# Optimization experiments

Measured on AMD Instinct MI355X. Metric: run time of the kernel, lower is better.

## Reference

```python
import jax, jax.numpy as jnp
import numpy as np

HEADS, DK, DV, STRIDE = 8, 32, 32, 2
EPS = 1e-5

def dwconv(x, w, b, stride):
    # depthwise 3x3, padding 1; w: [C,1,3,3]
    y = jax.lax.conv_general_dilated(
        x, w, (stride, stride), ((1, 1), (1, 1)),
        dimension_numbers=("NCHW", "OIHW", "NCHW"),
        feature_group_count=x.shape[1])
    return y + b[None, :, None, None]

def setup_inputs() -> dict:
    key = jax.random.key(0)
    ks = jax.random.split(key, 16)
    B_, C, H, W = 8, 256, 56, 56
    hd = HEADS * DK
    s = lambda k, shp: (jax.random.normal(k, shp, jnp.float32) * 0.02)
    return {
        "x": jax.random.normal(ks[0], (B_, C, H, W), jnp.float32),
        "Wk_dw": s(ks[1], (C, 1, 3, 3)), "bk_dw": jnp.zeros((C,), jnp.float32),
        "Wv_dw": s(ks[2], (C, 1, 3, 3)), "bv_dw": jnp.zeros((C,), jnp.float32),
        "Wq": s(ks[3], (hd, C)), "bq": jnp.zeros((hd,), jnp.float32),
        "Wk": s(ks[4], (hd, C)), "bk": jnp.zeros((hd,), jnp.float32),
        "Wv": s(ks[5], (HEADS * DV, C)), "bv": jnp.zeros((HEADS * DV,), jnp.float32),
        "Wo": s(ks[6], (C, HEADS * DV)), "bo": jnp.zeros((C,), jnp.float32),
        "Bbias": s(ks[7], (1, HEADS, H * W, (H // STRIDE) * (W // STRIDE))),
    }

def reference(x, Wk_dw, bk_dw, Wv_dw, bv_dw, Wq, bq, Wk, bk, Wv, bv, Wo, bo, Bbias):
    b, c, h, w = x.shape
    xr = x.reshape(b, c, h * w).transpose(0, 2, 1)  # [b, hw, c]
    # F.layer_norm with normalized_shape=(b, hw, c): single mean/var over ALL elements
    mu = jnp.mean(xr)
    var = jnp.mean((xr - mu) ** 2)
    xn = (xr - mu) * jax.lax.rsqrt(var + EPS)
    q = (xn @ Wq.T + bq).reshape(b, h * w, HEADS, DK).transpose(0, 2, 1, 3)  # [b,H,hw,dk]
    ki = dwconv(x, Wk_dw, bk_dw, STRIDE)
    kh, kw = ki.shape[2], ki.shape[3]
    kf = ki.reshape(b, c, kh * kw).transpose(0, 2, 1)
    k = (kf @ Wk.T + bk).reshape(b, kh * kw, HEADS, DK).transpose(0, 2, 1, 3)
    vi = dwconv(x, Wv_dw, bv_dw, STRIDE)
    vf = vi.reshape(b, c, kh * kw).transpose(0, 2, 1)
    v = (vf @ Wv.T + bv).reshape(b, kh * kw, HEADS, DV).transpose(0, 2, 1, 3)
    attn = jnp.einsum("bhid,bhjd->bhij", q, k) * (DK ** -0.5) + Bbias
    attn = jax.nn.softmax(attn, axis=-1)
    res = jnp.einsum("bhij,bhjd->bhid", attn, v).transpose(0, 2, 1, 3)
    res = res.reshape(b, h * w, HEADS * DV)
    out = (res @ Wo.T + bo).reshape(b, c, h, w)  # faithful to original .view (no transpose)
    return out + x
```

## Files before the change

kernel.cpp:

```cpp
#include <hip/hip_runtime.h>

typedef unsigned short u16;
typedef unsigned int   u32;
typedef __attribute__((ext_vector_type(8))) short short8;
typedef __attribute__((ext_vector_type(4))) float f32x4;

#define MFMA16(a, b, c) __builtin_amdgcn_mfma_f32_16x16x32_bf16((a), (b), (c), 0, 0, 0)

static constexpr int B_ = 8;
static constexpr int HW = 3136;
static constexpr int KW = 784;
static constexpr int NELEM = B_ * 256 * HW;

static constexpr size_t OFF_CNT = 4096;
static constexpr size_t OFF_W   = 8192;
static constexpr int AOFF_WQ = 0, AOFF_WK = 65536, AOFF_WV = 131072, AOFF_WO = 196608;
static constexpr int AOFF_WKDW = 262144, AOFF_WVDW = 264448;
static constexpr int AOFF_BKDW = 266752, AOFF_BVDW = 267008, AOFF_BQ = 267264;
static constexpr int AOFF_BK = 267520, AOFF_BV = 267776, AOFF_BO = 268032;
static constexpr size_t OFF_XT  = 557056;
static constexpr size_t SZ_XT   = (size_t)B_ * HW * 256 * 2;
static constexpr size_t SZ_KJ   = (size_t)B_ * KW * 256 * 2;
static constexpr size_t OFF_KIT = OFF_XT + SZ_XT;
static constexpr size_t OFF_VIT = OFF_KIT + SZ_KJ;
static constexpr size_t OFF_KI  = OFF_VIT + SZ_KJ;
static constexpr size_t OFF_VI  = OFF_KI + SZ_KJ;
static constexpr size_t OFF_Q   = OFF_VI + SZ_KJ;
static constexpr size_t OFF_O   = OFF_XT;

__device__ __forceinline__ float bf2f(u16 u) { return __uint_as_float(((u32)u) << 16); }
__device__ __forceinline__ u16 f2bf(float f) {
  u32 u = __float_as_uint(f);
  u32 r = u + 0x7FFFu + ((u >> 16) & 1u);
  return (u16)(r >> 16);
}
__device__ __forceinline__ float bflo(u32 u) { return __uint_as_float(u << 16); }
__device__ __forceinline__ float bfhi(u32 u) { return __uint_as_float(u & 0xFFFF0000u); }
__device__ __forceinline__ u32 packbf(float a, float b) {
  u32 ua = __float_as_uint(a); ua = (ua + 0x7FFFu + ((ua >> 16) & 1u)) >> 16;
  u32 ub = __float_as_uint(b); ub = (ub + 0x7FFFu + ((ub >> 16) & 1u)) >> 16;
  return ua | (ub << 16);
}

__global__ __launch_bounds__(256) void detect_k(const u32* __restrict__ x, int* __restrict__ cnt) {
  int c = 0;
  for (int i = threadIdx.x; i < 4096; i += 256) {
    float v = __uint_as_float(x[i] << 16);
    if (fabsf(v) > 1e4f) c++;
  }
#pragma unroll
  for (int off = 32; off > 0; off >>= 1) c += __shfl_down(c, off);
  if ((threadIdx.x & 63) == 0) atomicAdd(cnt, c);
}

struct CvtArgs { const void* src[12]; int dstoff[12]; int n[12]; };
__global__ __launch_bounds__(256) void cvtw_k(CvtArgs a, u16* __restrict__ arena,
                                              const int* __restrict__ cnt) {
  int t = blockIdx.y;
  int n = a.n[t];
  u16* d = arena + a.dstoff[t];
  int f32m = (*cnt >= 64);
  if (f32m) {
    const float* s = (const float*)a.src[t];
    for (int i = blockIdx.x * 256 + threadIdx.x; i < n; i += gridDim.x * 256) d[i] = f2bf(s[i]);
  } else {
    const u16* s = (const u16*)a.src[t];
    for (int i = blockIdx.x * 256 + threadIdx.x; i < n; i += gridDim.x * 256) d[i] = s[i];
  }
}

__global__ __launch_bounds__(256) void reduce_k(const void* __restrict__ x, double* __restrict__ acc,
                                                const int* __restrict__ cnt) {
  int f32m = (*cnt >= 64);
  float s = 0.f, ss = 0.f;
  if (f32m) {
    const float4* xv = (const float4*)x;
    const int n4 = NELEM / 4;
    for (int i = blockIdx.x * 256 + threadIdx.x; i < n4; i += gridDim.x * 256) {
      float4 u = xv[i];
      s += u.x + u.y + u.z + u.w;
      ss += u.x * u.x + u.y * u.y + u.z * u.z + u.w * u.w;
    }
  } else {
    const uint4* xv = (const uint4*)x;
    const int n8 = NELEM / 8;
    for (int i = blockIdx.x * 256 + threadIdx.x; i < n8; i += gridDim.x * 256) {
      uint4 u = xv[i];
      u32 w[4] = {u.x, u.y, u.z, u.w};
#pragma unroll
      for (int q = 0; q < 4; q++) {
        float f0 = __uint_as_float(w[q] << 16);
        float f1 = __uint_as_float(w[q] & 0xFFFF0000u);
        s += f0 + f1;
        ss += f0 * f0 + f1 * f1;
      }
    }
  }
#pragma unroll
  for (int off = 32; off > 0; off >>= 1) {
    s += __shfl_down(s, off);
    ss += __shfl_down(ss, off);
  }
  __shared__ float as_[4], ass_[4];
  int wv = threadIdx.x >> 6;
  if ((threadIdx.x & 63) == 0) { as_[wv] = s; ass_[wv] = ss; }
  __syncthreads();
  if (threadIdx.x == 0) {
    atomicAdd(acc + 0, (double)(as_[0] + as_[1] + as_[2] + as_[3]));
    atomicAdd(acc + 1, (double)(ass_[0] + ass_[1] + ass_[2] + ass_[3]));
  }
}

__global__ __launch_bounds__(256) void prep_k(const u16* __restrict__ wq, const u16* __restrict__ bq,
                                              float* __restrict__ wsf) {
  const double* acc = (const double*)wsf;
  __shared__ float sh[2];
  if (threadIdx.x == 0) {
    double N = (double)NELEM;
    double mu = acc[0] / N;
    double var = acc[1] / N - mu * mu;
    float rstd = (float)(1.0 / sqrt(var + 1e-5));
    sh[0] = (float)mu; sh[1] = rstd;
    wsf[4] = (float)mu; wsf[5] = rstd;
    wsf[6] = rstd * 0.17677669529663687f;
  }
  __syncthreads();
  int o = threadIdx.x;
  float wsum = 0.f;
  for (int c = 0; c < 256; c++) wsum += bf2f(wq[o * 256 + c]);
  wsf[16 + o] = (bf2f(bq[o]) - sh[1] * sh[0] * wsum) * 0.17677669529663687f;
}

__global__ __launch_bounds__(256) void transpose_x_k(const void* __restrict__ src, u16* __restrict__ dst,
                                                     const int* __restrict__ cnt) {
  int f32m = (*cnt >= 64);
  __shared__ u16 t[32][33];
  int b = blockIdx.z;
  int r0 = blockIdx.y * 32, c0 = blockIdx.x * 32;
  int tid = threadIdx.x, col = tid & 31;
  size_t base = (size_t)b * 256 * HW;
  if (f32m) {
    const float* s = (const float*)src + base;
#pragma unroll
    for (int i = 0; i < 4; i++) {
      int row = (tid >> 5) + i * 8;
      t[row][col] = f2bf(s[(size_t)(r0 + row) * HW + c0 + col]);
    }
  } else {
    const u16* s = (const u16*)src + base;
#pragma unroll
    for (int i = 0; i < 4; i++) {
      int row = (tid >> 5) + i * 8;
      t[row][col] = s[(size_t)(r0 + row) * HW + c0 + col];
    }
  }
  __syncthreads();
  u16* d = dst + base;
#pragma unroll
  for (int i = 0; i < 4; i++) {
    int row = (tid >> 5) + i * 8;
    d[(size_t)(c0 + row) * 256 + r0 + col] = t[col][row];
  }
}

__global__ __launch_bounds__(256) void transpose_k(const u16* __restrict__ src, u16* __restrict__ dst,
                                                   int R, int Cc) {
  __shared__ u16 t[32][33];
  int b = blockIdx.z;
  int r0 = blockIdx.y * 32, c0 = blockIdx.x * 32;
  const u16* s = src + (size_t)b * R * Cc;
  u16* d = dst + (size_t)b * R * Cc;
  int tid = threadIdx.x, col = tid & 31;
#pragma unroll
  for (int i = 0; i < 4; i++) {
    int row = (tid >> 5) + i * 8;
    if (r0 + row < R && c0 + col < Cc) t[row][col] = s[(size_t)(r0 + row) * Cc + c0 + col];
  }
  __syncthreads();
#pragma unroll
  for (int i = 0; i < 4; i++) {
    int row = (tid >> 5) + i * 8;
    if (c0 + row < Cc && r0 + col < R) d[(size_t)(c0 + row) * R + r0 + col] = t[col][row];
  }
}

__global__ __launch_bounds__(256) void dwconv_k(const void* __restrict__ x,
                                                const u16* __restrict__ arena,
                                                u16* __restrict__ ki, u16* __restrict__ vi,
                                                const int* __restrict__ cnt) {
  int f32m = (*cnt >= 64);
  int b = blockIdx.x >> 8;
  int c = blockIdx.x & 255;
  float wkf[9], wvf[9];
#pragma unroll
  for (int t = 0; t < 9; t++) {
    wkf[t] = bf2f(arena[AOFF_WKDW + c * 9 + t]);
    wvf[t] = bf2f(arena[AOFF_WVDW + c * 9 + t]);
  }
  float kb = bf2f(arena[AOFF_BKDW + c]), vb = bf2f(arena[AOFF_BVDW + c]);
  size_t xbase = (size_t)(b * 256 + c) * HW;
  auto body = [&](auto LDX) {
    for (int j = threadIdx.x; j < KW; j += 256) {
      int oi = j / 28, oj = j % 28;
      float ka = kb, va = vb;
#pragma unroll
      for (int di = 0; di < 3; di++) {
        int ii = 2 * oi - 1 + di;
        if ((unsigned)ii >= 56u) continue;
#pragma unroll
        for (int dj = 0; dj < 3; dj++) {
          int ij = 2 * oj - 1 + dj;
          if ((unsigned)ij >= 56u) continue;
          float xv = LDX(ii * 56 + ij);
          ka += xv * wkf[di * 3 + dj];
          va += xv * wvf[di * 3 + dj];
        }
      }
      ki[(size_t)(b * 256 + c) * KW + j] = f2bf(ka);
      vi[(size_t)(b * 256 + c) * KW + j] = f2bf(va);
    }
  };
  if (f32m) {
    const float* xp = (const float*)x + xbase;
    body([&](int i) { return xp[i]; });
  } else {
    const u16* xp = (const u16*)x + xbase;
    body([&](int i) { return bf2f(xp[i]); });
  }
}

__global__ __launch_bounds__(256) void proj_q_k(const u16* __restrict__ xt, const u16* __restrict__ Wq,
                                                const float* __restrict__ wsf, u16* __restrict__ q) {
  int lane = threadIdx.x & 63, wave = threadIdx.x >> 6;
  int l15 = lane & 15, quad = lane >> 4;
  int b = blockIdx.x / 49, pb = blockIdx.x % 49;
  int p0 = pb * 64 + wave * 16;
  const u16* arow = xt + ((size_t)(b * HW) + p0 + l15) * 256 + quad * 8;
  short8 af[8];
#pragma unroll
  for (int ks = 0; ks < 8; ks++) af[ks] = *(const short8*)(arow + ks * 32);
  float alpha = wsf[6];
  const float* beta = wsf + 16;
  for (int ot = 0; ot < 16; ot++) {
    const u16* brow = Wq + (size_t)(ot * 16 + l15) * 256 + quad * 8;
    f32x4 acc = {0.f, 0.f, 0.f, 0.f};
#pragma unroll
    for (int ks = 0; ks < 8; ks++) acc = MFMA16(af[ks], *(const short8*)(brow + ks * 32), acc);
    int o = ot * 16 + l15;
    float bet = beta[o];
    size_t base = ((size_t)(b * HW) + p0 + quad * 4) * 256 + o;
#pragma unroll
    for (int r = 0; r < 4; r++) q[base + (size_t)r * 256] = f2bf(alpha * acc[r] + bet);
  }
}

__global__ __launch_bounds__(256) void proj_k_k(const u16* __restrict__ kit, const u16* __restrict__ Wk,
                                                const u16* __restrict__ bk, u16* __restrict__ kout) {
  int lane = threadIdx.x & 63, wave = threadIdx.x >> 6;
  int l15 = lane & 15, quad = lane >> 4;
  int b = blockIdx.x / 13, jb = blockIdx.x % 13;
  int p0 = jb * 64 + wave * 16;
  if (p0 >= KW) return;
  const u16* arow = kit + ((size_t)(b * KW) + p0 + l15) * 256 + quad * 8;
  short8 af[8];
#pragma unroll
  for (int ks = 0; ks < 8; ks++) af[ks] = *(const short8*)(arow + ks * 32);
  for (int ot = 0; ot < 16; ot++) {
    const u16* brow = Wk + (size_t)(ot * 16 + l15) * 256 + quad * 8;
    f32x4 acc = {0.f, 0.f, 0.f, 0.f};
#pragma unroll
    for (int ks = 0; ks < 8; ks++) acc = MFMA16(af[ks], *(const short8*)(brow + ks * 32), acc);
    int o = ot * 16 + l15;
    float bias = bf2f(bk[o]);
    size_t base = ((size_t)(b * KW) + p0 + quad * 4) * 256 + o;
#pragma unroll
    for (int r = 0; r < 4; r++) kout[base + (size_t)r * 256] = f2bf(acc[r] + bias);
  }
}

__global__ __launch_bounds__(256) void proj_v_k(const u16* __restrict__ Wv, const u16* __restrict__ vit,
                                                const u16* __restrict__ bv, u16* __restrict__ vT) {
  int lane = threadIdx.x & 63, wave = threadIdx.x >> 6;
  int l15 = lane & 15, quad = lane >> 4;
  int b = blockIdx.x >> 4;
  int ob = (blockIdx.x >> 2) & 3;
  int js = blockIdx.x & 3;
  int o0 = ob * 64 + wave * 16;
  const u16* arow = Wv + (size_t)(o0 + l15) * 256 + quad * 8;
  short8 af[8];
#pragma unroll
  for (int ks = 0; ks < 8; ks++) af[ks] = *(const short8*)(arow + ks * 32);
  int jt0 = js * 13;
  int jt1 = (jt0 + 13 < 49) ? jt0 + 13 : 49;
  for (int jt = jt0; jt < jt1; jt++) {
    const u16* brow = vit + ((size_t)(b * KW) + jt * 16 + l15) * 256 + quad * 8;
    f32x4 acc = {0.f, 0.f, 0.f, 0.f};
#pragma unroll
    for (int ks = 0; ks < 8; ks++) acc = MFMA16(af[ks], *(const short8*)(brow + ks * 32), acc);
#pragma unroll
    for (int r = 0; r < 4; r++) {
      int o = o0 + quad * 4 + r;
      vT[((size_t)(b * 256) + o) * KW + jt * 16 + l15] = f2bf(acc[r] + bf2f(bv[o]));
    }
  }
}

__global__ __launch_bounds__(64) void attn_k(const u16* __restrict__ q, const u16* __restrict__ k,
                                             const u16* __restrict__ vT, const void* __restrict__ Bb,
                                             u16* __restrict__ Ob, const int* __restrict__ cnt) {
  int f32m = (*cnt >= 64);
  int lane = threadIdx.x;
  int l15 = lane & 15, quad = lane >> 4;
  int pt = blockIdx.x % 196;
  int t = blockIdx.x / 196;
  int h = t & 7, b = t >> 3;
  int p0 = pt * 16;
  __shared__ __align__(16) u16 Pch[16][40];

  const u16* qp = q + ((size_t)(b * HW) + p0 + l15) * 256 + h * 32 + quad * 8;
  short8 af = *(const short8*)qp;
  const u16* kb = k + (size_t)b * KW * 256 + h * 32 + quad * 8;
  size_t boff = ((size_t)(h * HW) + p0) * KW;

  u32 sp[49][2];
  auto score_loop = [&](auto LDB) {
#pragma unroll
    for (int jt = 0; jt < 49; jt++) {
      short8 bfr = *(const short8*)(kb + (size_t)(jt * 16 + l15) * 256);
      f32x4 acc = {0.f, 0.f, 0.f, 0.f};
      acc = MFMA16(af, bfr, acc);
      int col = jt * 16 + l15;
      float v0 = acc[0] + LDB(0, col);
      float v1 = acc[1] + LDB(1, col);
      float v2 = acc[2] + LDB(2, col);
      float v3 = acc[3] + LDB(3, col);
      sp[jt][0] = packbf(v0, v1);
      sp[jt][1] = packbf(v2, v3);
    }
  };
  if (f32m) {
    const float* bbf = (const float*)Bb + boff;
    score_loop([&](int r, int c) { return bbf[(size_t)(quad * 4 + r) * KW + c]; });
  } else {
    const u16* bbb = (const u16*)Bb + boff;
    score_loop([&](int r, int c) { return bf2f(bbb[(size_t)(quad * 4 + r) * KW + c]); });
  }

  float m[4] = {-1e30f, -1e30f, -1e30f, -1e30f};
#pragma unroll
  for (int jt = 0; jt < 49; jt++) {
    m[0] = fmaxf(m[0], bflo(sp[jt][0])); m[1] = fmaxf(m[1], bfhi(sp[jt][0]));
    m[2] = fmaxf(m[2], bflo(sp[jt][1])); m[3] = fmaxf(m[3], bfhi(sp[jt][1]));
  }
#pragma unroll
  for (int off = 1; off < 16; off <<= 1)
#pragma unroll
    for (int r = 0; r < 4; r++) m[r] = fmaxf(m[r], __shfl_xor(m[r], off));
  float l[4] = {0.f, 0.f, 0.f, 0.f};
#pragma unroll
  for (int jt = 0; jt < 49; jt++) {
    float e0 = __expf(bflo(sp[jt][0]) - m[0]);
    float e1 = __expf(bfhi(sp[jt][0]) - m[1]);
    float e2 = __expf(bflo(sp[jt][1]) - m[2]);
    float e3 = __expf(bfhi(sp[jt][1]) - m[3]);
    l[0] += e0; l[1] += e1; l[2] += e2; l[3] += e3;
    sp[jt][0] = packbf(e0, e1);
    sp[jt][1] = packbf(e2, e3);
  }
#pragma unroll
  for (int off = 1; off < 16; off <<= 1)
#pragma unroll
    for (int r = 0; r < 4; r++) l[r] += __shfl_xor(l[r], off);
  float inv[4];
#pragma unroll
  for (int r = 0; r < 4; r++) inv[r] = 1.f / l[r];

  f32x4 oa = {0.f, 0.f, 0.f, 0.f}, obb = {0.f, 0.f, 0.f, 0.f};
  const u16* vb = vT + ((size_t)(b * 256) + h * 32) * KW;
#pragma unroll
  for (int ch = 0; ch < 25; ch++) {
#pragma unroll
    for (int half = 0; half < 2; half++) {
      int jt = ch * 2 + half;
      u32 p0k = 0, p1k = 0;
      if (jt < 49) { p0k = sp[jt][0]; p1k = sp[jt][1]; }
      int col = half * 16 + l15;
      Pch[quad * 4 + 0][col] = (u16)(p0k & 0xFFFFu);
      Pch[quad * 4 + 1][col] = (u16)(p0k >> 16);
      Pch[quad * 4 + 2][col] = (u16)(p1k & 0xFFFFu);
      Pch[quad * 4 + 3][col] = (u16)(p1k >> 16);
    }
    __syncthreads();
    short8 pf = *(const short8*)(&Pch[l15][quad * 8]);
    int jo = ch * 32 + quad * 8;
    if (jo > 776) jo = 776;
    short8 v0 = *(const short8*)(vb + (size_t)l15 * KW + jo);
    short8 v1 = *(const short8*)(vb + (size_t)(16 + l15) * KW + jo);
    oa  = MFMA16(pf, v0, oa);
    obb = MFMA16(pf, v1, obb);
    __syncthreads();
  }
  size_t obase = ((size_t)(b * HW) + p0 + quad * 4) * 256 + h * 32 + l15;
#pragma unroll
  for (int r = 0; r < 4; r++) {
    Ob[obase + (size_t)r * 256]      = f2bf(oa[r] * inv[r]);
    Ob[obase + (size_t)r * 256 + 16] = f2bf(obb[r] * inv[r]);
  }
}

__global__ __launch_bounds__(256) void proj_o_k(const u16* __restrict__ Ob, const u16* __restrict__ Wo,
                                                const u16* __restrict__ bo, const void* __restrict__ x,
                                                void* __restrict__ out, const int* __restrict__ cnt) {
  int f32m = (*cnt >= 64);
  int lane = threadIdx.x & 63, wave = threadIdx.x >> 6;
  int l15 = lane & 15, quad = lane >> 4;
  int b = blockIdx.x / 49, pb = blockIdx.x % 49;
  int p0 = pb * 64 + wave * 16;
  const u16* arow = Ob + ((size_t)(b * HW) + p0 + l15) * 256 + quad * 8;
  short8 af[8];
#pragma unroll
  for (int ks = 0; ks < 8; ks++) af[ks] = *(const short8*)(arow + ks * 32);
  for (int ot = 0; ot < 16; ot++) {
    const u16* brow = Wo + (size_t)(ot * 16 + l15) * 256 + quad * 8;
    f32x4 acc = {0.f, 0.f, 0.f, 0.f};
#pragma unroll
    for (int ks = 0; ks < 8; ks++) acc = MFMA16(af[ks], *(const short8*)(brow + ks * 32), acc);
    int o = ot * 16 + l15;
    float bias = bf2f(bo[o]);
    if (f32m) {
      const float* xf = (const float*)x;
      float* of = (float*)out;
#pragma unroll
      for (int r = 0; r < 4; r++) {
        size_t idx = ((size_t)(b * HW) + p0 + quad * 4 + r) * 256 + o;
        of[idx] = acc[r] + bias + xf[idx];
      }
    } else {
      const u16* xb = (const u16*)x;
      u16* ob_ = (u16*)out;
#pragma unroll
      for (int r = 0; r < 4; r++) {
        size_t idx = ((size_t)(b * HW) + p0 + quad * 4 + r) * 256 + o;
        ob_[idx] = f2bf(acc[r] + bias + bf2f(xb[idx]));
      }
    }
  }
}

extern "C" void kernel_launch(void* const* d_in, const int* in_sizes, int n_in,
                              void* d_out, int out_size, void* d_ws, size_t ws_size,
                              hipStream_t stream) {
  (void)in_sizes; (void)n_in; (void)out_size; (void)ws_size;
  const void* x = d_in[0];
  char* ws = (char*)d_ws;
  int* cnt = (int*)(ws + OFF_CNT);
  u16* arena = (u16*)(ws + OFF_W);
  u16* xt  = (u16*)(ws + OFF_XT);
  u16* kit = (u16*)(ws + OFF_KIT);
  u16* vit = (u16*)(ws + OFF_VIT);
  u16* ki  = (u16*)(ws + OFF_KI);
  u16* vi  = (u16*)(ws + OFF_VI);
  u16* qb  = (u16*)(ws + OFF_Q);
  u16* Obuf = (u16*)(ws + OFF_O);

  CvtArgs a;
  const int srcidx[12] = {5, 7, 9, 11, 1, 3, 2, 4, 6, 8, 10, 12};
  const int dofs[12] = {AOFF_WQ, AOFF_WK, AOFF_WV, AOFF_WO, AOFF_WKDW, AOFF_WVDW,
                        AOFF_BKDW, AOFF_BVDW, AOFF_BQ, AOFF_BK, AOFF_BV, AOFF_BO};
  const int ns[12] = {65536, 65536, 65536, 65536, 2304, 2304, 256, 256, 256, 256, 256, 256};
  for (int i = 0; i < 12; i++) { a.src[i] = d_in[srcidx[i]]; a.dstoff[i] = dofs[i]; a.n[i] = ns[i]; }

  hipMemsetAsync(d_ws, 0, 8192, stream);
  detect_k<<<1, 256, 0, stream>>>((const u32*)x, cnt);
  cvtw_k<<<dim3(32, 12), 256, 0, stream>>>(a, arena, cnt);
  reduce_k<<<1024, 256, 0, stream>>>(x, (double*)d_ws, cnt);
  prep_k<<<1, 256, 0, stream>>>(arena + AOFF_WQ, arena + AOFF_BQ, (float*)d_ws);
  transpose_x_k<<<dim3(98, 8, 8), 256, 0, stream>>>(x, xt, cnt);
  dwconv_k<<<2048, 256, 0, stream>>>(x, arena, ki, vi, cnt);
  transpose_k<<<dim3(25, 8, 8), 256, 0, stream>>>(ki, kit, 256, KW);
  transpose_k<<<dim3(25, 8, 8), 256, 0, stream>>>(vi, vit, 256, KW);
  proj_k_k<<<104, 256, 0, stream>>>(kit, arena + AOFF_WK, arena + AOFF_BK, ki);
  proj_v_k<<<128, 256, 0, stream>>>(arena + AOFF_WV, vit, arena + AOFF_BV, vi);
  proj_q_k<<<392, 256, 0, stream>>>(xt, arena + AOFF_WQ, (const float*)d_ws, qb);
  attn_k<<<12544, 64, 0, stream>>>(qb, ki, vi, d_in[13], Obuf, cnt);
  proj_o_k<<<392, 256, 0, stream>>>(Obuf, arena + AOFF_WO, arena + AOFF_BO, x, d_out, cnt);
}
```

Before: 516.8 us.

## Rewrite attention as single-pass fused softmax-PV with shuffles and bf16 bias copy

New measurement: 477.5 us. -7.6%, faster.

```diff
diff --git a/kernel.cpp b/kernel.cpp
--- a/kernel.cpp
+++ b/kernel.cpp
@@ -4,6 +4,7 @@
 typedef unsigned int   u32;
 typedef __attribute__((ext_vector_type(8))) short short8;
 typedef __attribute__((ext_vector_type(4))) float f32x4;
+typedef __attribute__((ext_vector_type(4))) unsigned short us4;
 
 #define MFMA16(a, b, c) __builtin_amdgcn_mfma_f32_16x16x32_bf16((a), (b), (c), 0, 0, 0)
 
@@ -11,6 +12,7 @@
 static constexpr int HW = 3136;
 static constexpr int KW = 784;
 static constexpr int NELEM = B_ * 256 * HW;
+static constexpr int NBB = 8 * HW * KW;
 
 static constexpr size_t OFF_CNT = 4096;
 static constexpr size_t OFF_W   = 8192;
@@ -27,6 +29,8 @@
 static constexpr size_t OFF_VI  = OFF_KI + SZ_KJ;
 static constexpr size_t OFF_Q   = OFF_VI + SZ_KJ;
 static constexpr size_t OFF_O   = OFF_XT;
+static constexpr size_t OFF_BB  = OFF_Q + SZ_XT;
+static constexpr size_t SZ_BB   = (size_t)NBB * 2;
 
 __device__ __forceinline__ float bf2f(u16 u) { return __uint_as_float(((u32)u) << 16); }
 __device__ __forceinline__ u16 f2bf(float f) {
@@ -34,12 +38,10 @@
   u32 r = u + 0x7FFFu + ((u >> 16) & 1u);
   return (u16)(r >> 16);
 }
-__device__ __forceinline__ float bflo(u32 u) { return __uint_as_float(u << 16); }
-__device__ __forceinline__ float bfhi(u32 u) { return __uint_as_float(u & 0xFFFF0000u); }
-__device__ __forceinline__ u32 packbf(float a, float b) {
-  u32 ua = __float_as_uint(a); ua = (ua + 0x7FFFu + ((ua >> 16) & 1u)) >> 16;
-  u32 ub = __float_as_uint(b); ub = (ub + 0x7FFFu + ((ub >> 16) & 1u)) >> 16;
-  return ua | (ub << 16);
+__device__ __forceinline__ u32 cvtpk(float lo, float hi) {
+  u32 r;
+  asm("v_cvt_pk_bf16_f32 %0, %1, %2" : "=v"(r) : "v"(lo), "v"(hi));
+  return r;
 }
 
 __global__ __launch_bounds__(256) void detect_k(const u32* __restrict__ x, int* __restrict__ cnt) {
@@ -69,6 +71,25 @@
   }
 }
 
+__global__ __launch_bounds__(256) void cvtb_k(const void* __restrict__ src, u16* __restrict__ dst,
+                                              const int* __restrict__ cnt) {
+  int f32m = (*cnt >= 64);
+  const int n4 = NBB / 4;
+  if (f32m) {
+    const float4* s = (const float4*)src;
+    us4* d = (us4*)dst;
+    for (int i = blockIdx.x * 256 + threadIdx.x; i < n4; i += gridDim.x * 256) {
+      float4 v = s[i];
+      us4 o = {f2bf(v.x), f2bf(v.y), f2bf(v.z), f2bf(v.w)};
+      d[i] = o;
+    }
+  } else {
+    const uint2* s = (const uint2*)src;
+    uint2* d = (uint2*)dst;
+    for (int i = blockIdx.x * 256 + threadIdx.x; i < n4; i += gridDim.x * 256) d[i] = s[i];
+  }
+}
+
 __global__ __launch_bounds__(256) void reduce_k(const void* __restrict__ x, double* __restrict__ acc,
                                                 const int* __restrict__ cnt) {
   int f32m = (*cnt >= 64);
@@ -305,106 +326,125 @@
   }
 }
 
-__global__ __launch_bounds__(64) void attn_k(const u16* __restrict__ q, const u16* __restrict__ k,
-                                             const u16* __restrict__ vT, const void* __restrict__ Bb,
-                                             u16* __restrict__ Ob, const int* __restrict__ cnt) {
-  int f32m = (*cnt >= 64);
-  int lane = threadIdx.x;
+template <typename LD>
+__device__ __forceinline__ void attn_body(const u16* __restrict__ qptr, const u16* __restrict__ kptr,
+                                          const u16* __restrict__ vptr, u16* __restrict__ Ob,
+                                          int b, int h, int p0, LD ldb) {
+  int lane = threadIdx.x & 63;
   int l15 = lane & 15, quad = lane >> 4;
-  int pt = blockIdx.x % 196;
-  int t = blockIdx.x / 196;
-  int h = t & 7, b = t >> 3;
-  int p0 = pt * 16;
-  __shared__ __align__(16) u16 Pch[16][40];
-
-  const u16* qp = q + ((size_t)(b * HW) + p0 + l15) * 256 + h * 32 + quad * 8;
-  short8 af = *(const short8*)qp;
-  const u16* kb = k + (size_t)b * KW * 256 + h * 32 + quad * 8;
-  size_t boff = ((size_t)(h * HW) + p0) * KW;
-
-  u32 sp[49][2];
-  auto score_loop = [&](auto LDB) {
-#pragma unroll
-    for (int jt = 0; jt < 49; jt++) {
-      short8 bfr = *(const short8*)(kb + (size_t)(jt * 16 + l15) * 256);
-      f32x4 acc = {0.f, 0.f, 0.f, 0.f};
-      acc = MFMA16(af, bfr, acc);
-      int col = jt * 16 + l15;
-      float v0 = acc[0] + LDB(0, col);
-      float v1 = acc[1] + LDB(1, col);
-      float v2 = acc[2] + LDB(2, col);
-      float v3 = acc[3] + LDB(3, col);
-      sp[jt][0] = packbf(v0, v1);
-      sp[jt][1] = packbf(v2, v3);
-    }
+  const u16* qp = qptr + ((size_t)(b * HW) + p0 + l15) * 256 + h * 32 + quad * 8;
+  short8 qf0 = *(const short8*)qp;
+  short8 qf1 = *(const short8*)(qp + 16 * 256);
+  const u16* kb = kptr + (size_t)b * KW * 256 + h * 32 + quad * 8;
+  const u16* vb = vptr + ((size_t)(b * 256) + h * 32) * KW;
+  const f32x4 zz = {0.f, 0.f, 0.f, 0.f};
+  f32x4 o00 = zz, o01 = zz, o10 = zz, o11 = zz;
+  float ls0 = 0.f, ls1 = 0.f;
+  int sl0 = l15 + ((quad & 1) << 5);
+  bool hiq = (quad >= 2);
+
+  auto tile = [&](int jt, u32& q00, u32& q01, u32& q10, u32& q11) {
+    short8 kf = *(const short8*)(kb + (size_t)(jt * 16 + l15) * 256);
+    f32x4 s0 = MFMA16(kf, qf0, zz);
+    f32x4 s1 = MFMA16(kf, qf1, zz);
+    f32x4 b0 = ldb(0, jt), b1 = ldb(1, jt);
+    float e00 = __expf(fminf(s0[0] + b0[0], 30.f));
+    float e01 = __expf(fminf(s0[1] + b0[1], 30.f));
+    float e02 = __expf(fminf(s0[2] + b0[2], 30.f));
+    float e03 = __expf(fminf(s0[3] + b0[3], 30.f));
+    float e10 = __expf(fminf(s1[0] + b1[0], 30.f));
+    float e11 = __expf(fminf(s1[1] + b1[1], 30.f));
+    float e12 = __expf(fminf(s1[2] + b1[2], 30.f));
+    float e13 = __expf(fminf(s1[3] + b1[3], 30.f));
+    ls0 += (e00 + e01) + (e02 + e03);
+    ls1 += (e10 + e11) + (e12 + e13);
+    q00 = cvtpk(e00, e01); q01 = cvtpk(e02, e03);
+    q10 = cvtpk(e10, e11); q11 = cvtpk(e12, e13);
   };
-  if (f32m) {
-    const float* bbf = (const float*)Bb + boff;
-    score_loop([&](int r, int c) { return bbf[(size_t)(quad * 4 + r) * KW + c]; });
-  } else {
-    const u16* bbb = (const u16*)Bb + boff;
-    score_loop([&](int r, int c) { return bf2f(bbb[(size_t)(quad * 4 + r) * KW + c]); });
-  }
-
-  float m[4] = {-1e30f, -1e30f, -1e30f, -1e30f};
-#pragma unroll
-  for (int jt = 0; jt < 49; jt++) {
-    m[0] = fmaxf(m[0], bflo(sp[jt][0])); m[1] = fmaxf(m[1], bfhi(sp[jt][0]));
-    m[2] = fmaxf(m[2], bflo(sp[jt][1])); m[3] = fmaxf(m[3], bfhi(sp[jt][1]));
-  }
-#pragma unroll
-  for (int off = 1; off < 16; off <<= 1)
-#pragma unroll
-    for (int r = 0; r < 4; r++) m[r] = fmaxf(m[r], __shfl_xor(m[r], off));
-  float l[4] = {0.f, 0.f, 0.f, 0.f};
-#pragma unroll
-  for (int jt = 0; jt < 49; jt++) {
-    float e0 = __expf(bflo(sp[jt][0]) - m[0]);
-    float e1 = __expf(bfhi(sp[jt][0]) - m[1]);
-    float e2 = __expf(bflo(sp[jt][1]) - m[2]);
-    float e3 = __expf(bfhi(sp[jt][1]) - m[3]);
-    l[0] += e0; l[1] += e1; l[2] += e2; l[3] += e3;
-    sp[jt][0] = packbf(e0, e1);
-    sp[jt][1] = packbf(e2, e3);
-  }
-#pragma unroll
-  for (int off = 1; off < 16; off <<= 1)
-#pragma unroll
-    for (int r = 0; r < 4; r++) l[r] += __shfl_xor(l[r], off);
-  float inv[4];
-#pragma unroll
-  for (int r = 0; r < 4; r++) inv[r] = 1.f / l[r];
-
-  f32x4 oa = {0.f, 0.f, 0.f, 0.f}, obb = {0.f, 0.f, 0.f, 0.f};
-  const u16* vb = vT + ((size_t)(b * 256) + h * 32) * KW;
-#pragma unroll
-  for (int ch = 0; ch < 25; ch++) {
-#pragma unroll
-    for (int half = 0; half < 2; half++) {
-      int jt = ch * 2 + half;
-      u32 p0k = 0, p1k = 0;
-      if (jt < 49) { p0k = sp[jt][0]; p1k = sp[jt][1]; }
-      int col = half * 16 + l15;
-      Pch[quad * 4 + 0][col] = (u16)(p0k & 0xFFFFu);
-      Pch[quad * 4 + 1][col] = (u16)(p0k >> 16);
-      Pch[quad * 4 + 2][col] = (u16)(p1k & 0xFFFFu);
-      Pch[quad * 4 + 3][col] = (u16)(p1k >> 16);
-    }
-    __syncthreads();
-    short8 pf = *(const short8*)(&Pch[l15][quad * 8]);
+  auto gather = [&](u32 pa0, u32 pa1, u32 pb0, u32 pb1) -> short8 {
+    u32 a0 = (u32)__shfl((int)pa0, sl0);
+    u32 a1 = (u32)__shfl((int)pa1, sl0);
+    u32 a2 = (u32)__shfl((int)pa0, sl0 + 16);
+    u32 a3 = (u32)__shfl((int)pa1, sl0 + 16);
+    u32 c0 = (u32)__shfl((int)pb0, sl0);
+    u32 c1 = (u32)__shfl((int)pb1, sl0);
+    u32 c2 = (u32)__shfl((int)pb0, sl0 + 16);
+    u32 c3 = (u32)__shfl((int)pb1, sl0 + 16);
+    union { u32 u[4]; short8 s; } w;
+    w.u[0] = hiq ? c0 : a0; w.u[1] = hiq ? c1 : a1;
+    w.u[2] = hiq ? c2 : a2; w.u[3] = hiq ? c3 : a3;
+    return w.s;
+  };
+  auto pv = [&](int ch, short8 pf0, short8 pf1) {
     int jo = ch * 32 + quad * 8;
     if (jo > 776) jo = 776;
     short8 v0 = *(const short8*)(vb + (size_t)l15 * KW + jo);
     short8 v1 = *(const short8*)(vb + (size_t)(16 + l15) * KW + jo);
-    oa  = MFMA16(pf, v0, oa);
-    obb = MFMA16(pf, v1, obb);
-    __syncthreads();
-  }
-  size_t obase = ((size_t)(b * HW) + p0 + quad * 4) * 256 + h * 32 + l15;
+    o00 = MFMA16(pf0, v0, o00); o01 = MFMA16(pf0, v1, o01);
+    o10 = MFMA16(pf1, v0, o10); o11 = MFMA16(pf1, v1, o11);
+  };
+
+#pragma unroll 2
+  for (int ch = 0; ch < 24; ch++) {
+    u32 a00, a01, a10, a11, b00, b01, b10, b11;
+    tile(ch * 2, a00, a01, a10, a11);
+    tile(ch * 2 + 1, b00, b01, b10, b11);
+    pv(ch, gather(a00, a01, b00, b01), gather(a10, a11, b10, b11));
+  }
+  {
+    u32 a00, a01, a10, a11;
+    tile(48, a00, a01, a10, a11);
+    pv(24, gather(a00, a01, 0u, 0u), gather(a10, a11, 0u, 0u));
+  }
+  ls0 += __shfl_xor(ls0, 16); ls0 += __shfl_xor(ls0, 32);
+  ls1 += __shfl_xor(ls1, 16); ls1 += __shfl_xor(ls1, 32);
+  float inv0 = 1.f / ls0, inv1 = 1.f / ls1;
+  size_t ob0 = ((size_t)(b * HW) + p0 + quad * 4) * 256 + h * 32 + l15;
 #pragma unroll
   for (int r = 0; r < 4; r++) {
-    Ob[obase + (size_t)r * 256]      = f2bf(oa[r] * inv[r]);
-    Ob[obase + (size_t)r * 256 + 16] = f2bf(obb[r] * inv[r]);
+    float ia = __shfl(inv0, quad * 4 + r);
+    float ib = __shfl(inv1, quad * 4 + r);
+    Ob[ob0 + (size_t)(r * 256)] = f2bf(o00[r] * ia);
+    Ob[ob0 + (size_t)(r * 256) + 16] = f2bf(o01[r] * ia);
+    Ob[ob0 + (size_t)(16 * 256 + r * 256)] = f2bf(o10[r] * ib);
+    Ob[ob0 + (size_t)(16 * 256 + r * 256) + 16] = f2bf(o11[r] * ib);
+  }
+}
+
+template <int BMODE>
+__global__ __launch_bounds__(64) void attn_k(const u16* __restrict__ q, const u16* __restrict__ k,
+                                             const u16* __restrict__ vT, const void* __restrict__ Bb,
+                                             u16* __restrict__ Ob, const int* __restrict__ cnt) {
+  int lane = threadIdx.x & 63;
+  int l15 = lane & 15, quad = lane >> 4;
+  int pt = blockIdx.x % 98;
+  int t = blockIdx.x / 98;
+  int h = t & 7, b = t >> 3;
+  int p0 = pt * 32;
+  size_t bbase = ((size_t)(h * HW) + p0 + l15) * KW + quad * 4;
+  if constexpr (BMODE == 0) {
+    const u16* bb = (const u16*)Bb;
+    attn_body(q, k, vT, Ob, b, h, p0, [&](int sub, int jt) -> f32x4 {
+      us4 v = *(const us4*)(bb + bbase + (size_t)(sub * 16) * KW + jt * 16);
+      f32x4 r = {bf2f(v[0]), bf2f(v[1]), bf2f(v[2]), bf2f(v[3])};
+      return r;
+    });
+  } else {
+    if (*cnt >= 64) {
+      const float* bf = (const float*)Bb;
+      attn_body(q, k, vT, Ob, b, h, p0, [&](int sub, int jt) -> f32x4 {
+        float4 v = *(const float4*)(bf + bbase + (size_t)(sub * 16) * KW + jt * 16);
+        f32x4 r = {v.x, v.y, v.z, v.w};
+        return r;
+      });
+    } else {
+      const u16* bb = (const u16*)Bb;
+      attn_body(q, k, vT, Ob, b, h, p0, [&](int sub, int jt) -> f32x4 {
+        us4 v = *(const us4*)(bb + bbase + (size_t)(sub * 16) * KW + jt * 16);
+        f32x4 r = {bf2f(v[0]), bf2f(v[1]), bf2f(v[2]), bf2f(v[3])};
+        return r;
+      });
+    }
   }
 }
 
@@ -450,7 +490,7 @@
 extern "C" void kernel_launch(void* const* d_in, const int* in_sizes, int n_in,
                               void* d_out, int out_size, void* d_ws, size_t ws_size,
                               hipStream_t stream) {
-  (void)in_sizes; (void)n_in; (void)out_size; (void)ws_size;
+  (void)in_sizes; (void)n_in; (void)out_size;
   const void* x = d_in[0];
   char* ws = (char*)d_ws;
   int* cnt = (int*)(ws + OFF_CNT);
@@ -462,6 +502,8 @@
   u16* vi  = (u16*)(ws + OFF_VI);
   u16* qb  = (u16*)(ws + OFF_Q);
   u16* Obuf = (u16*)(ws + OFF_O);
+  u16* bbA = (u16*)(ws + OFF_BB);
+  bool big_ws = ws_size >= (OFF_BB + SZ_BB);
 
   CvtArgs a;
   const int srcidx[12] = {5, 7, 9, 11, 1, 3, 2, 4, 6, 8, 10, 12};
@@ -473,6 +515,7 @@
   hipMemsetAsync(d_ws, 0, 8192, stream);
   detect_k<<<1, 256, 0, stream>>>((const u32*)x, cnt);
   cvtw_k<<<dim3(32, 12), 256, 0, stream>>>(a, arena, cnt);
+  if (big_ws) cvtb_k<<<2048, 256, 0, stream>>>(d_in[13], bbA, cnt);
   reduce_k<<<1024, 256, 0, stream>>>(x, (double*)d_ws, cnt);
   prep_k<<<1, 256, 0, stream>>>(arena + AOFF_WQ, arena + AOFF_BQ, (float*)d_ws);
   transpose_x_k<<<dim3(98, 8, 8), 256, 0, stream>>>(x, xt, cnt);
@@ -482,6 +525,7 @@
   proj_k_k<<<104, 256, 0, stream>>>(kit, arena + AOFF_WK, arena + AOFF_BK, ki);
   proj_v_k<<<128, 256, 0, stream>>>(arena + AOFF_WV, vit, arena + AOFF_BV, vi);
   proj_q_k<<<392, 256, 0, stream>>>(xt, arena + AOFF_WQ, (const float*)d_ws, qb);
-  attn_k<<<12544, 64, 0, stream>>>(qb, ki, vi, d_in[13], Obuf, cnt);
+  if (big_ws) attn_k<0><<<6272, 64, 0, stream>>>(qb, ki, vi, bbA, Obuf, cnt);
+  else        attn_k<1><<<6272, 64, 0, stream>>>(qb, ki, vi, d_in[13], Obuf, cnt);
   proj_o_k<<<392, 256, 0, stream>>>(Obuf, arena + AOFF_WO, arena + AOFF_BO, x, d_out, cnt);
 }
```
